# Kernel optimization log

Hardware: AMD Instinct MI355X
Metric: run time of the kernel (lower is better)

## Reference

```python
import jax, jax.numpy as jnp
import numpy as np

E = 1024; H = 16; L = 4; V = 32000; FF = 4096
B = 2; NX = 1023; S = 1024
EPS = 1e-5


def _pe(n_pos, d):
    # sinusoidal table; original registers pe of shape [max_len, 1, d]
    pos = np.arange(n_pos, dtype=np.float32)[:, None]
    div = np.exp(np.arange(0, d, 2, dtype=np.float32) * (-np.log(10000.0) / d))
    pe = np.zeros((n_pos, d), dtype=np.float32)
    pe[:, 0::2] = np.sin(pos * div)
    pe[:, 1::2] = np.cos(pos * div)
    return jnp.asarray(pe)


def _ln(x, g, b):
    m = jnp.mean(x, -1, keepdims=True)
    v = jnp.mean((x - m) ** 2, -1, keepdims=True)
    return (x - m) / jnp.sqrt(v + EPS) * g + b


def _mha(q, k, v, Wq, bq, Wk, bk, Wv, bv, Wo, bo, mask=None):
    b, lq, e = q.shape
    hd = e // H
    qh = (q @ Wq + bq).reshape(b, lq, H, hd)
    kh = (k @ Wk + bk).reshape(b, k.shape[1], H, hd)
    vh = (v @ Wv + bv).reshape(b, v.shape[1], H, hd)
    s = jnp.einsum('bqhe,bkhe->bhqk', qh, kh)
    if mask is not None:
        s = jnp.where(mask == 0, -1e9, s)  # mask applied BEFORE scaling, as in source
    s = s / np.float32(np.sqrt(e))        # quirk: scaled by sqrt(embed_size), not head_size
    a = jax.nn.softmax(s, axis=-1)
    o = jnp.einsum('bhqk,bkhd->bqhd', a, vh).reshape(b, lq, e)
    return o @ Wo + bo


def _forward(emb, cls, sWq, sbq, sWk, sbk, sWv, sbv, sWo, sbo,
             cWq, cbq, cWk, cbk, cWv, cbv, cWo, cbo,
             g1, b1, g2, b2, g3, b3, fW1, fb1, fW2, fb2, x_tok, y_tok):
    scale = np.float32(np.sqrt(E))
    # quirk: original adds pe[:x.size(0)] (batch dim!) broadcast over sequence
    pe = _pe(x_tok.shape[0], E)
    x = emb[x_tok] * scale + pe[:, None, :]
    y = emb[y_tok] * scale + pe[:, None, :]
    s = y_tok.shape[1]
    mask = jnp.tril(jnp.ones((s, s), jnp.float32))[None, None]  # [1,1,s,s] causal
    x = jnp.concatenate([x, jnp.broadcast_to(cls, (x.shape[0], 1, E))], axis=1)
    for l in range(L):
        # quirk: every layer self-attends over the ORIGINAL embedded y
        a1 = _mha(y, y, y, sWq[l], sbq[l], sWk[l], sbk[l], sWv[l], sbv[l], sWo[l], sbo[l], mask)
        yl = _ln(y + a1, g1[l], b1[l])
        a2 = _mha(yl, x, x, cWq[l], cbq[l], cWk[l], cbk[l], cWv[l], cbv[l], cWo[l], cbo[l])
        x = _ln(yl + a2, g2[l], b2[l])
        h = jax.nn.relu(x @ fW1[l] + fb1[l]) @ fW2[l] + fb2[l]
        x = _ln(x + h, g3[l], b3[l])
    return x


def setup_inputs() -> dict:
    key = jax.random.key(0)
    specs = [('emb', (V, E), 1.0), ('cls', (1, 1, E), 1.0),
             ('sWq', (L, E, E), 0.02), ('sbq', (L, E), 0.01), ('sWk', (L, E, E), 0.02), ('sbk', (L, E), 0.01),
             ('sWv', (L, E, E), 0.02), ('sbv', (L, E), 0.01), ('sWo', (L, E, E), 0.02), ('sbo', (L, E), 0.01),
             ('cWq', (L, E, E), 0.02), ('cbq', (L, E), 0.01), ('cWk', (L, E, E), 0.02), ('cbk', (L, E), 0.01),
             ('cWv', (L, E, E), 0.02), ('cbv', (L, E), 0.01), ('cWo', (L, E, E), 0.02), ('cbo', (L, E), 0.01),
             ('fW1', (L, E, FF), 0.02), ('fb1', (L, FF), 0.01), ('fW2', (L, FF, E), 0.02), ('fb2', (L, E), 0.01)]
    d = {}
    for i, (n, sh, sc) in enumerate(specs):
        d[n] = jax.random.normal(jax.random.fold_in(key, i), sh, jnp.float32) * sc
    for n in ('g1', 'g2', 'g3'):
        d[n] = jnp.ones((L, E), jnp.float32)
    for n in ('b1', 'b2', 'b3'):
        d[n] = jnp.zeros((L, E), jnp.float32)
    d['x_tok'] = jax.random.randint(jax.random.fold_in(key, 100), (B, NX), 0, V)
    d['y_tok'] = jax.random.randint(jax.random.fold_in(key, 101), (B, S), 0, V)
    return d


def reference(x_tok, y_tok, emb, cls, sWq, sbq, sWk, sbk, sWv, sbv, sWo, sbo,
              cWq, cbq, cWk, cbk, cWv, cbv, cWo, cbo,
              g1, b1, g2, b2, g3, b3, fW1, fb1, fW2, fb2):
    return _forward(emb, cls, sWq, sbq, sWk, sbk, sWv, sbv, sWo, sbo,
                    cWq, cbq, cWk, cbk, cWv, cbv, cWo, cbo,
                    g1, b1, g2, b2, g3, b3, fW1, fb1, fW2, fb2, x_tok, y_tok)
```

## Files before the change

kernel.cpp:

```cpp
#include <hip/hip_runtime.h>
#include <cstdint>

#define ESZ 1024
#define NH 16
#define HD 64
#define NLAYER 4
#define FFD 4096
#define NB 2
#define NXTOK 1023
#define SEQ 1024
#define LNEPS 1e-5f

typedef __attribute__((ext_vector_type(8))) _Float16 f16x8;
typedef __attribute__((ext_vector_type(4))) _Float16 f16x4;
typedef __attribute__((ext_vector_type(4))) float f32x4;

__device__ __forceinline__ void gld16(const void* g, void* l) {
  __builtin_amdgcn_global_load_lds(
      (const __attribute__((address_space(1))) unsigned int*)g,
      (__attribute__((address_space(3))) unsigned int*)l, 16, 0, 0);
}

__device__ __forceinline__ uint3 xcd_swz() {
  unsigned gx = gridDim.x, gy = gridDim.y;
  unsigned nwg = gx * gy * gridDim.z;
  unsigned lin = (blockIdx.z * gy + blockIdx.y) * gx + blockIdx.x;
  unsigned q = nwg >> 3, r = nwg & 7;
  unsigned xcd = lin & 7, idx = lin >> 3;
  unsigned wid = (xcd < r ? xcd * (q + 1) : r * (q + 1) + (xcd - r) * q) + idx;
  uint3 o;
  o.x = wid % gx;
  unsigned t = wid / gx;
  o.y = t % gy;
  o.z = t / gy;
  return o;
}

template<int MI, int NJ, int EPI, bool RELU, int SPLITK>
__device__ __forceinline__ void gemm_epi(
    f32x4 (&acc)[MI][NJ], int m0, int n0, int wr, int wc, int lr, int hi,
    int z, size_t coff, int ldc,
    const float* bias0, const float* bias1, const float* bias2, int bstr,
    void* C0, void* C1, long sC1, long sC2, int vseg)
{
  const int rb = hi * 4;
#pragma unroll
  for (int j = 0; j < NJ; j++) {
    const int n = n0 + wc + j * 16 + lr;
    float bv = 0.f;
    if (EPI == 2) {
      int seg = n >> 10;
      const float* bp = (seg == 0) ? bias0 : ((seg == 1) ? bias1 : bias2);
      bv = bp[bstr * z + (n & 1023)];
    } else if (bias0) bv = bias0[bstr * z + n];
    if (SPLITK > 1 && z > 0) bv = 0.f;
#pragma unroll
    for (int i = 0; i < MI; i++) {
#pragma unroll
      for (int r = 0; r < 4; r++) {
        int row = m0 + wr + i * 16 + rb + r;
        float out = acc[i][j][r] + bv;
        if (RELU) out = fmaxf(out, 0.f);
        if (EPI == 0) {
          ((float*)C0)[coff + (size_t)row * ldc + n] = out;
        } else if (EPI == 1) {
          ((_Float16*)C0)[coff + (size_t)row * ldc + n] = (_Float16)out;
        } else {
          int seg = n >> 10, n1 = n & 1023, h = n1 >> 6, d = n1 & 63;
          int b = row >> 10, s = row & 1023;
          if (seg == vseg)
            ((_Float16*)C1)[(size_t)z * sC2 + (((size_t)b * NH + h) * HD + d) * SEQ + s] = (_Float16)out;
          else
            ((_Float16*)C0)[(size_t)z * sC1 + (size_t)seg * ((size_t)NB * NH * SEQ * HD)
                            + (((size_t)b * NH + h) * SEQ + s) * HD + d] = (_Float16)out;
        }
      }
    }
  }
}

template<int BM, int BN, int EPI, bool RELU, int SPLITK>
__global__ __launch_bounds__(256)
void gemm_k(const _Float16* __restrict__ A, const _Float16* __restrict__ Bm,
            const float* __restrict__ bias0, const float* __restrict__ bias1,
            const float* __restrict__ bias2,
            void* __restrict__ C0, void* __restrict__ C1,
            int K, int lda, int ldb, int ldc,
            long sAz, long sBz, int cdiv, long sC1, long sC2, int vseg, int bstr)
{
  constexpr int MI = BM / 32, NJ = BN / 32;
  constexpr int DBUF = 2 * (BM + BN) * 64;
  constexpr int TBUF = (EPI == 2) ? 128 * 136 : 0;
  constexpr int LDSN = (TBUF > DBUF) ? TBUF : DBUF;
  __shared__ _Float16 lds[LDSN];

  const uint3 bi = xcd_swz();
  const int m0 = bi.x * BM;
  const int n0 = bi.y * BN;
  const int z = bi.z;
  const _Float16* Ab;
  const _Float16* Bb;
  size_t coff;
  if (SPLITK > 1) {
    int koff = z * (K / SPLITK);
    Ab = A + koff;
    Bb = Bm + koff;
    coff = (size_t)z * sC1;
  } else {
    Ab = A + (size_t)z * sAz;
    Bb = Bm + (size_t)z * sBz;
    coff = (size_t)(z / cdiv) * sC1 + (size_t)(z % cdiv) * sC2;
  }
  const int tid = threadIdx.x;
  const int lane = tid & 63;
  const int w = tid >> 6;
  const int lr = lane & 15;
  const int hi = lane >> 4;
  const int wr = (w >> 1) * (BM / 2);
  const int wc = (w & 1) * (BN / 2);

  const f32x4 vz = {0.f, 0.f, 0.f, 0.f};
  f32x4 acc[MI][NJ];
#pragma unroll
  for (int i = 0; i < MI; i++)
#pragma unroll
    for (int j = 0; j < NJ; j++) acc[i][j] = vz;

  const int nk = (K / SPLITK) >> 6;

  auto stage = [&](int buf, int kt) {
    const int k0 = kt << 6;
    _Float16* Ah = lds + buf * (BM * 64);
    _Float16* Bh = lds + 2 * (BM * 64) + buf * (BN * 64);
#pragma unroll
    for (int c = 0; c < MI; c++) {
      int r = w * (BM / 4) + c * 8 + (lane >> 3);
      int cg = ((lane & 7) ^ (r & 7)) << 3;
      gld16(Ab + (size_t)(m0 + r) * lda + k0 + cg, Ah + (w * (BM / 4) + c * 8) * 64);
    }
#pragma unroll
    for (int c = 0; c < NJ; c++) {
      int r = w * (BN / 4) + c * 8 + (lane >> 3);
      int cg = ((lane & 7) ^ (r & 7)) << 3;
      gld16(Bb + (size_t)(n0 + r) * ldb + k0 + cg, Bh + (w * (BN / 4) + c * 8) * 64);
    }
  };

  stage(0, 0);
  int cur = 0;
  for (int kt = 0; kt < nk; ++kt) {
    __syncthreads();
    if (kt + 1 < nk) stage(cur ^ 1, kt + 1);
    const char* Ah = (const char*)(lds + cur * (BM * 64));
    const char* Bh = (const char*)(lds + 2 * (BM * 64) + cur * (BN * 64));
#pragma unroll
    for (int kk = 0; kk < 2; kk++) {
      f16x8 af[MI], bf[NJ];
#pragma unroll
      for (int i = 0; i < MI; i++) {
        int row = wr + i * 16 + lr;
        int off = ((kk << 6) | (hi << 4)) ^ ((row & 7) << 4);
        af[i] = *(const f16x8*)(Ah + row * 128 + off);
      }
#pragma unroll
      for (int j = 0; j < NJ; j++) {
        int row = wc + j * 16 + lr;
        int off = ((kk << 6) | (hi << 4)) ^ ((row & 7) << 4);
        bf[j] = *(const f16x8*)(Bh + row * 128 + off);
      }
#pragma unroll
      for (int i = 0; i < MI; i++)
#pragma unroll
        for (int j = 0; j < NJ; j++)
          acc[i][j] = __builtin_amdgcn_mfma_f32_16x16x32_f16(af[i], bf[j], acc[i][j], 0, 0, 0);
    }
    cur ^= 1;
  }

  if (EPI == 2 && (n0 >> 10) == vseg) {
    __syncthreads();
    _Float16* T = lds;
    const float* bp = (vseg == 0) ? bias0 : ((vseg == 1) ? bias1 : bias2);
#pragma unroll
    for (int j = 0; j < NJ; j++) {
      int nloc = wc + j * 16 + lr;
      float bv = bp[bstr * z + ((n0 + nloc) & 1023)];
#pragma unroll
      for (int i = 0; i < MI; i++) {
        f16x4 tv;
#pragma unroll
        for (int r = 0; r < 4; r++) tv[r] = (_Float16)(acc[i][j][r] + bv);
        *(f16x4*)(T + nloc * 136 + wr + i * 16 + hi * 4) = tv;
      }
    }
    __syncthreads();
    int rowT = tid >> 1;
    int c0 = (tid & 1) << 6;
    int nn = (n0 & 1023) + rowT;
    int h = nn >> 6, d = nn & 63;
    int bb = m0 >> 10;
    int s0 = (m0 & 1023) + c0;
    _Float16* dst = (_Float16*)C1 + (size_t)z * sC2
                  + (((size_t)bb * NH + h) * HD + d) * SEQ + s0;
    const _Float16* src = T + rowT * 136 + c0;
#pragma unroll
    for (int t2 = 0; t2 < 8; t2++)
      *(f16x8*)(dst + t2 * 8) = *(const f16x8*)(src + t2 * 8);
    return;
  }

  gemm_epi<MI, NJ, EPI, RELU, SPLITK>(acc, m0, n0, wr, wc, lr, hi, z, coff, ldc,
                                      bias0, bias1, bias2, bstr, C0, C1, sC1, sC2, vseg);
}

template<bool CAUSAL>
__global__ __launch_bounds__(256)
void flash_k(const _Float16* __restrict__ qh, const _Float16* __restrict__ kh,
             const _Float16* __restrict__ vTp, _Float16* __restrict__ ob,
             long qs, long ks, long vs, long os)
{
  __shared__ _Float16 Kl[2][64 * 64];
  __shared__ _Float16 Vl[2][64 * 64];
  const uint3 bi = xcd_swz();
  const int qb = bi.x;
  const int bh = bi.y;
  const int layer = bi.z;
  const int b = bh >> 4, h = bh & 15;
  const int q0 = qb * 128;
  const int tid = threadIdx.x;
  const int w = tid >> 6, lane = tid & 63;
  const int lr = lane & 15, hi = lane >> 4;
  const int qw = q0 + w * 32;

  const _Float16* Qp = qh + (size_t)layer * qs + (size_t)bh * SEQ * HD;
  const _Float16* Kp = kh + (size_t)layer * ks + (size_t)bh * SEQ * HD;
  const _Float16* Vp = vTp + (size_t)layer * vs + (size_t)bh * HD * SEQ;
  ob += (size_t)layer * os;

  f16x8 qf[2][2];
#pragma unroll
  for (int jq = 0; jq < 2; jq++)
#pragma unroll
    for (int ds = 0; ds < 2; ds++)
      qf[jq][ds] = *(const f16x8*)(Qp + (size_t)(qw + jq * 16 + lr) * HD + ds * 32 + hi * 8);

  float m[2] = {-1e30f, -1e30f}, l[2] = {0.f, 0.f};
  const f32x4 vz = {0.f, 0.f, 0.f, 0.f};
  f32x4 o[4][2];
#pragma unroll
  for (int dt = 0; dt < 4; dt++)
#pragma unroll
    for (int jq = 0; jq < 2; jq++) o[dt][jq] = vz;

  const int nst = CAUSAL ? ((q0 >> 6) + 2) : (SEQ / 64);

  auto stage = [&](int buf, int kt) {
    const int k0 = kt << 6;
#pragma unroll
    for (int c = 0; c < 2; c++) {
      int r = w * 16 + c * 8 + (lane >> 3);
      int cg = ((lane & 7) ^ (r & 7)) << 3;
      gld16(Kp + (size_t)(k0 + r) * HD + cg, &Kl[buf][(w * 16 + c * 8) * 64]);
      gld16(Vp + (size_t)r * SEQ + k0 + cg, &Vl[buf][(w * 16 + c * 8) * 64]);
    }
  };

  stage(0, 0);
  int cur = 0;
  for (int kt = 0; kt < nst; ++kt) {
    __syncthreads();
    if (kt + 1 < nst) stage(cur ^ 1, kt + 1);
    const int k0 = kt << 6;
    if (!CAUSAL || k0 <= qw + 31) {
      f32x4 s[4][2];
#pragma unroll
      for (int ik = 0; ik < 4; ik++)
#pragma unroll
        for (int jq = 0; jq < 2; jq++) s[ik][jq] = vz;
#pragma unroll
      for (int ds = 0; ds < 2; ds++) {
        f16x8 kf[4];
#pragma unroll
        for (int ik = 0; ik < 4; ik++) {
          int row = ik * 16 + lr;
          int off = (ds * 64 + hi * 16) ^ ((row & 7) << 4);
          kf[ik] = *(const f16x8*)((const char*)&Kl[cur][0] + row * 128 + off);
        }
        __builtin_amdgcn_s_setprio(1);
#pragma unroll
        for (int ik = 0; ik < 4; ik++)
#pragma unroll
          for (int jq = 0; jq < 2; jq++)
            s[ik][jq] = __builtin_amdgcn_mfma_f32_16x16x32_f16(kf[ik], qf[jq][ds], s[ik][jq], 0, 0, 0);
        __builtin_amdgcn_s_setprio(0);
      }
      float mx[2] = {-1e30f, -1e30f};
#pragma unroll
      for (int ik = 0; ik < 4; ik++)
#pragma unroll
        for (int jq = 0; jq < 2; jq++)
#pragma unroll
          for (int r = 0; r < 4; r++) {
            float v = s[ik][jq][r] * 0.03125f;
            if (CAUSAL) {
              int kk = k0 + ik * 16 + hi * 4 + r;
              int qq = qw + jq * 16 + lr;
              if (kk > qq) v = -1e30f;
            }
            s[ik][jq][r] = v;
            mx[jq] = fmaxf(mx[jq], v);
          }
      float sc[2], cs[2] = {0.f, 0.f};
      f16x4 pb[4][2];
#pragma unroll
      for (int jq = 0; jq < 2; jq++) {
        mx[jq] = fmaxf(mx[jq], __shfl_xor(mx[jq], 16, 64));
        mx[jq] = fmaxf(mx[jq], __shfl_xor(mx[jq], 32, 64));
        float mn = fmaxf(m[jq], mx[jq]);
        sc[jq] = __expf(m[jq] - mn);
        m[jq] = mn;
      }
#pragma unroll
      for (int ik = 0; ik < 4; ik++)
#pragma unroll
        for (int jq = 0; jq < 2; jq++)
#pragma unroll
          for (int r = 0; r < 4; r++) {
            float p = __expf(s[ik][jq][r] - m[jq]);
            cs[jq] += p;
            pb[ik][jq][r] = (_Float16)p;
          }
#pragma unroll
      for (int jq = 0; jq < 2; jq++) {
        float t = cs[jq];
        t += __shfl_xor(t, 16, 64);
        t += __shfl_xor(t, 32, 64);
        l[jq] = l[jq] * sc[jq] + t;
      }
#pragma unroll
      for (int dt = 0; dt < 4; dt++)
#pragma unroll
        for (int jq = 0; jq < 2; jq++)
#pragma unroll
          for (int r = 0; r < 4; r++) o[dt][jq][r] *= sc[jq];
#pragma unroll
      for (int ks2 = 0; ks2 < 4; ks2++) {
        f16x4 va[4];
#pragma unroll
        for (int dt = 0; dt < 4; dt++) {
          int row = dt * 16 + lr;
          int off = (ks2 * 32 + hi * 8) ^ ((row & 7) << 4);
          va[dt] = *(const f16x4*)((const char*)&Vl[cur][0] + row * 128 + off);
        }
        __builtin_amdgcn_s_setprio(1);
#pragma unroll
        for (int dt = 0; dt < 4; dt++)
#pragma unroll
          for (int jq = 0; jq < 2; jq++)
            o[dt][jq] = __builtin_amdgcn_mfma_f32_16x16x16f16(va[dt], pb[ks2][jq], o[dt][jq], 0, 0, 0);
        __builtin_amdgcn_s_setprio(0);
      }
    }
    cur ^= 1;
  }

  float inv[2] = {1.f / l[0], 1.f / l[1]};
#pragma unroll
  for (int jq = 0; jq < 2; jq++) {
    int q = qw + jq * 16 + lr;
    size_t rowoff = (size_t)(b * SEQ + q) * ESZ + h * 64;
#pragma unroll
    for (int dt = 0; dt < 4; dt++) {
      f16x4 ov;
#pragma unroll
      for (int r = 0; r < 4; r++) ov[r] = (_Float16)(o[dt][jq][r] * inv[jq]);
      *(f16x4*)(ob + rowoff + dt * 16 + hi * 4) = ov;
    }
  }
}

__device__ __forceinline__ void wtr4(const float* __restrict__ src,
                                     _Float16* __restrict__ dst,
                                     int K, int Ns, int k0, int n0, int tid,
                                     float* T )
{
  const int w = tid >> 6, lane = tid & 63;
#pragma unroll
  for (int rr = 0; rr < 8; rr++) {
    int r = w * 8 + rr;
    const float* s = src + (size_t)(k0 + r) * Ns + n0;
    gld16(s + lane * 4, T + r * 512);
    gld16(s + 256 + lane * 4, T + r * 512 + 256);
  }
  __syncthreads();
#pragma unroll
  for (int pass = 0; pass < 2; pass++) {
    int n = pass * 256 + tid;
    float vv[32];
#pragma unroll
    for (int kk = 0; kk < 32; kk++) vv[kk] = T[kk * 512 + n];
    _Float16* d = dst + (size_t)(n0 + n) * K + k0;
#pragma unroll
    for (int c = 0; c < 4; c++) {
      f16x8 o;
#pragma unroll
      for (int i = 0; i < 8; i++) o[i] = (_Float16)vv[c * 8 + i];
      *(f16x8*)(d + c * 8) = o;
    }
  }
  __syncthreads();
}

struct W8 { const float* p[8]; };

__global__ __launch_bounds__(256)
void prep_k(W8 w8, const float* __restrict__ fW1, const float* __restrict__ fW2,
            _Float16* __restrict__ W16,
            const int* __restrict__ xt, const int* __restrict__ yt,
            const float* __restrict__ emb, const float* __restrict__ cls,
            float* __restrict__ y32, _Float16* __restrict__ y16,
            _Float16* __restrict__ x16)
{
  __shared__ float T[32 * 512];
  const size_t MM = (size_t)1 << 20;
  int idx = blockIdx.x;
  int tid = threadIdx.x;
  if (idx < 2048) {
    int z = idx >> 6, rem = idx & 63;
    int widx = z >> 2, layer = z & 3;
    const float* src = w8.p[widx] + (size_t)layer * (ESZ * ESZ);
    _Float16* dst = W16 + (size_t)layer * 16 * MM + (size_t)widx * MM;
    wtr4(src, dst, 1024, 1024, (rem & 31) * 32, (rem >> 5) * 512, tid, T);
    return;
  }
  if (idx < 3072) {
    int i = idx - 2048;
    int z = i >> 8, rem = i & 255;
    wtr4(fW1 + (size_t)z * ESZ * FFD, W16 + (size_t)z * 16 * MM + 8 * MM,
         1024, 4096, (rem & 31) * 32, (rem >> 5) * 512, tid, T);
    return;
  }
  if (idx < 4096) {
    int i = idx - 3072;
    int z = i >> 8, rem = i & 255;
    wtr4(fW2 + (size_t)z * ESZ * FFD, W16 + (size_t)z * 16 * MM + 12 * MM,
         4096, 1024, (rem & 127) * 32, (rem >> 7) * 512, tid, T);
    return;
  }
  int row = idx - 4096;
  bool isx = row < NB * SEQ;
  int rr = isx ? row : row - NB * SEQ;
  int b = rr >> 10, tpos = rr & (SEQ - 1);
  int col0 = tid * 4;
  float v[4];
  if (isx && tpos == SEQ - 1) {
#pragma unroll
    for (int j = 0; j < 4; j++) v[j] = cls[col0 + j];
  } else {
    int tok = isx ? xt[b * NXTOK + tpos] : yt[b * SEQ + tpos];
    const float* erow = emb + (size_t)tok * ESZ;
#pragma unroll
    for (int j = 0; j < 4; j++) {
      int e = col0 + j;
      float div = expf((float)(e & ~1) * (-9.210340371976184f / 1024.f));
      float ang = (float)b * div;
      float pe = (e & 1) ? cosf(ang) : sinf(ang);
      v[j] = erow[e] * 32.f + pe;
    }
  }
  size_t off = (size_t)rr * ESZ + col0;
  if (isx) {
#pragma unroll
    for (int j = 0; j < 4; j++) x16[off + j] = (_Float16)v[j];
  } else {
#pragma unroll
    for (int j = 0; j < 4; j++) { y32[off + j] = v[j]; y16[off + j] = (_Float16)v[j]; }
  }
}

template<int NP>
__global__ __launch_bounds__(256)
void lnres_k(const float* __restrict__ a, const _Float16* __restrict__ r0,
             const _Float16* __restrict__ r1, const _Float16* __restrict__ r2,
             const _Float16* __restrict__ r3,
             const float* __restrict__ g, const float* __restrict__ b,
             float* __restrict__ o32, _Float16* __restrict__ o16,
             long aStr, long rStr, long oStr, int gStr)
{
  int row = blockIdx.x;
  int lz = blockIdx.y;
  a += (size_t)lz * aStr;
  r0 += (size_t)lz * rStr;
  o32 += (size_t)lz * oStr;
  o16 += (size_t)lz * oStr;
  g += (size_t)lz * gStr;
  b += (size_t)lz * gStr;
  size_t off = (size_t)row * ESZ;
  int tid = threadIdx.x;
  float4 va = *(const float4*)(a + off + tid * 4);
  float x[4] = {va.x, va.y, va.z, va.w};
  {
    f16x4 v = *(const f16x4*)(r0 + off + tid * 4);
#pragma unroll
    for (int j = 0; j < 4; j++) x[j] += (float)v[j];
  }
  if (NP >= 2) {
    f16x4 v = *(const f16x4*)(r1 + off + tid * 4);
#pragma unroll
    for (int j = 0; j < 4; j++) x[j] += (float)v[j];
  }
  if (NP >= 4) {
    f16x4 v = *(const f16x4*)(r2 + off + tid * 4);
    f16x4 u = *(const f16x4*)(r3 + off + tid * 4);
#pragma unroll
    for (int j = 0; j < 4; j++) x[j] += (float)v[j] + (float)u[j];
  }
  float s = x[0] + x[1] + x[2] + x[3];
  float s2 = x[0] * x[0] + x[1] * x[1] + x[2] * x[2] + x[3] * x[3];
  for (int o = 32; o > 0; o >>= 1) {
    s += __shfl_xor(s, o, 64);
    s2 += __shfl_xor(s2, o, 64);
  }
  __shared__ float rs[4], rs2[4];
  if ((tid & 63) == 0) { rs[tid >> 6] = s; rs2[tid >> 6] = s2; }
  __syncthreads();
  s = rs[0] + rs[1] + rs[2] + rs[3];
  s2 = rs2[0] + rs2[1] + rs2[2] + rs2[3];
  float mean = s * (1.f / ESZ);
  float var = s2 * (1.f / ESZ) - mean * mean;
  float inv = 1.f / sqrtf(var + LNEPS);
  float4 vo;
#pragma unroll
  for (int j = 0; j < 4; j++) {
    int c = tid * 4 + j;
    float o = (x[j] - mean) * inv * g[c] + b[c];
    ((float*)&vo)[j] = o;
    o16[off + c] = (_Float16)o;
  }
  *(float4*)(o32 + off + tid * 4) = vo;
}


template<int BM, int BN, int EPI, bool RELU, int SPLITK>
static void gemm(hipStream_t st, const _Float16* A, const _Float16* B,
                 const float* b0, const float* b1, const float* b2,
                 void* C0, void* C1, int M, int N, int K,
                 int lda, int ldb, int ldc,
                 int Z, long sAz, long sBz, int cdiv, long sC1, long sC2,
                 int vseg, int bstr)
{
  dim3 g(M / BM, N / BN, Z);
  gemm_k<BM, BN, EPI, RELU, SPLITK><<<g, dim3(256), 0, st>>>(
      A, B, b0, b1, b2, C0, C1, K, lda, ldb, ldc, sAz, sBz, cdiv, sC1, sC2, vseg, bstr);
}

extern "C" void kernel_launch(void* const* d_in, const int* in_sizes, int n_in,
                              void* d_out, int out_size, void* d_ws, size_t ws_size,
                              hipStream_t stream) {
  (void)n_in; (void)out_size; (void)ws_size;
  const float *emb, *cls, *sWq, *sbq, *sWk, *sbk, *sWv, *sbv, *sWo, *sbo;
  const float *cWq, *cbq, *cWk, *cbk, *cWv, *cbv, *cWo, *cbo;
  const float *fW1, *fb1, *fW2, *fb2, *g1, *g2, *g3, *b1, *b2, *b3;
  const int *xt, *yt;
  if (in_sizes[0] == NB * NXTOK) {
    xt = (const int*)d_in[0]; yt = (const int*)d_in[1];
    emb = (const float*)d_in[2]; cls = (const float*)d_in[3];
    sWq = (const float*)d_in[4]; sbq = (const float*)d_in[5];
    sWk = (const float*)d_in[6]; sbk = (const float*)d_in[7];
    sWv = (const float*)d_in[8]; sbv = (const float*)d_in[9];
    sWo = (const float*)d_in[10]; sbo = (const float*)d_in[11];
    cWq = (const float*)d_in[12]; cbq = (const float*)d_in[13];
    cWk = (const float*)d_in[14]; cbk = (const float*)d_in[15];
    cWv = (const float*)d_in[16]; cbv = (const float*)d_in[17];
    cWo = (const float*)d_in[18]; cbo = (const float*)d_in[19];
    g1 = (const float*)d_in[20]; b1 = (const float*)d_in[21];
    g2 = (const float*)d_in[22]; b2 = (const float*)d_in[23];
    g3 = (const float*)d_in[24]; b3 = (const float*)d_in[25];
    fW1 = (const float*)d_in[26]; fb1 = (const float*)d_in[27];
    fW2 = (const float*)d_in[28]; fb2 = (const float*)d_in[29];
  } else {
    emb = (const float*)d_in[0]; cls = (const float*)d_in[1];
    sWq = (const float*)d_in[2]; sbq = (const float*)d_in[3];
    sWk = (const float*)d_in[4]; sbk = (const float*)d_in[5];
    sWv = (const float*)d_in[6]; sbv = (const float*)d_in[7];
    sWo = (const float*)d_in[8]; sbo = (const float*)d_in[9];
    cWq = (const float*)d_in[10]; cbq = (const float*)d_in[11];
    cWk = (const float*)d_in[12]; cbk = (const float*)d_in[13];
    cWv = (const float*)d_in[14]; cbv = (const float*)d_in[15];
    cWo = (const float*)d_in[16]; cbo = (const float*)d_in[17];
    fW1 = (const float*)d_in[18]; fb1 = (const float*)d_in[19];
    fW2 = (const float*)d_in[20]; fb2 = (const float*)d_in[21];
    g1 = (const float*)d_in[22]; g2 = (const float*)d_in[23]; g3 = (const float*)d_in[24];
    b1 = (const float*)d_in[25]; b2 = (const float*)d_in[26]; b3 = (const float*)d_in[27];
    xt = (const int*)d_in[28]; yt = (const int*)d_in[29];
  }

  const size_t MM = (size_t)1 << 20;
  _Float16* W16 = (_Float16*)d_ws;
  _Float16* qhk_all = W16 + 64 * MM;
  _Float16* vT_all  = W16 + 80 * MM;
  _Float16* ob_all  = W16 + 88 * MM;
  _Float16* y16     = W16 + 96 * MM;
  _Float16* yl16_all= W16 + 98 * MM;
  _Float16* cqh_all = W16 + 106 * MM;
  _Float16* kh_c    = W16 + 114 * MM;
  _Float16* vT_c    = W16 + 116 * MM;
  _Float16* ob_c    = W16 + 118 * MM;
  _Float16* x16     = W16 + 120 * MM;
  _Float16* ffn     = W16 + 122 * MM;
  float* y32      = (float*)(W16 + 130 * MM);
  _Float16* tmp16 = (_Float16*)(y32 + 2 * MM);
  float* yl32_all = y32 + 10 * MM;
  float* x32      = y32 + 18 * MM;
  const long SP16 = 2048L * 1024;

  W8 w8;
  w8.p[0] = sWq; w8.p[1] = sWk; w8.p[2] = sWv; w8.p[3] = cWq;
  w8.p[4] = cWk; w8.p[5] = cWv; w8.p[6] = sWo; w8.p[7] = cWo;
  prep_k<<<dim3(8192), 256, 0, stream>>>(w8, fW1, fW2, W16, xt, yt, emb, cls,
                                         y32, y16, x16);

  gemm<128, 128, 2, false, 1>(stream, y16, W16, sbq, sbk, sbv,
      qhk_all, vT_all, 2048, 3072, 1024, 1024, 1024, 0,
      4, 0, 16 * MM, 1, 4 * MM, 2 * MM, 2, 1024);
  flash_k<true><<<dim3(8, 32, 4), 256, 0, stream>>>(
      qhk_all, qhk_all + 2 * MM, vT_all, ob_all, 4 * MM, 4 * MM, 2 * MM, 2 * MM);
  gemm<128, 128, 1, false, 1>(stream, ob_all, W16 + 6 * MM, sbo, nullptr, nullptr,
      tmp16, nullptr, 2048, 1024, 1024, 1024, 1024, 1024,
      4, 2 * MM, 16 * MM, 1, SP16, 0, 0, 1024);
  lnres_k<1><<<dim3(2048, 4), 256, 0, stream>>>(y32, tmp16, nullptr, nullptr, nullptr,
      g1, b1, yl32_all, yl16_all, 0, SP16, 2 * MM, 1024);
  gemm<128, 128, 2, false, 1>(stream, yl16_all, W16 + 3 * MM, cbq, nullptr, nullptr,
      cqh_all, nullptr, 2048, 1024, 1024, 1024, 1024, 0,
      4, 2 * MM, 16 * MM, 1, 2 * MM, 0, 3, 1024);

  for (int l = 0; l < NLAYER; l++) {
    _Float16* wl   = W16 + (size_t)l * 16 * MM;
    _Float16* wckv = wl + 4 * MM;
    _Float16* wco  = wl + 7 * MM;
    _Float16* wf1  = wl + 8 * MM;
    _Float16* wf2  = wl + 12 * MM;

    gemm<128, 128, 2, false, 1>(stream, x16, wckv, cbk + l * ESZ, cbv + l * ESZ,
        nullptr, kh_c, vT_c, 2048, 2048, 1024, 1024, 1024, 0,
        1, 0, 0, 1, 0, 0, 1, 0);
    flash_k<false><<<dim3(8, 32, 1), 256, 0, stream>>>(
        cqh_all + (size_t)l * 2 * MM, kh_c, vT_c, ob_c, 0, 0, 0, 0);
    gemm<128, 128, 1, false, 2>(stream, ob_c, wco, cbo + l * ESZ, nullptr, nullptr,
        tmp16, nullptr, 2048, 1024, 1024, 1024, 1024, 1024,
        2, 0, 0, 1, SP16, 0, 0, 0);
    lnres_k<2><<<dim3(2048, 1), 256, 0, stream>>>(yl32_all + (size_t)l * 2 * MM,
        tmp16, tmp16 + SP16, nullptr, nullptr,
        g2 + l * ESZ, b2 + l * ESZ, x32, x16, 0, 0, 0, 0);

    gemm<128, 128, 1, true, 1>(stream, x16, wf1, fb1 + l * FFD, nullptr, nullptr,
        ffn, nullptr, 2048, 4096, 1024, 1024, 1024, 4096,
        1, 0, 0, 1, 0, 0, 0, 0);
    gemm<128, 128, 1, false, 4>(stream, ffn, wf2, fb2 + l * ESZ, nullptr, nullptr,
        tmp16, nullptr, 2048, 1024, 4096, 4096, 4096, 1024,
        4, 0, 0, 1, SP16, 0, 0, 0);
    lnres_k<4><<<dim3(2048, 1), 256, 0, stream>>>(x32, tmp16, tmp16 + SP16,
        tmp16 + 2 * SP16, tmp16 + 3 * SP16, g3 + l * ESZ, b3 + l * ESZ,
        (l == NLAYER - 1) ? (float*)d_out : x32, x16, 0, 0, 0, 0);
  }
}
```

Before: 814.9 us.

## Pre-tile transposed fp16 weights into contiguous 128x64 blocks for GEMM B loads

The weight-prep kernel now writes each transposed fp16 weight as contiguous 128(N)x64(K) tiles, so each 64-wide K step of a GEMM block's B operand is one 16 KB contiguous chunk. The GEMM B-stage addressing is changed to match this blocked layout, including the split-K offset. This is meant to make B global loads fully sequential and simplify prep-kernel transposes with smaller LDS tiles, at the cost of more prep blocks. The layout assumes BN=128 and would break for other B tile widths or for any GEMM whose B operand is not a pre-tiled weight.

```diff
diff --git a/kernel.cpp b/kernel.cpp
--- a/kernel.cpp
+++ b/kernel.cpp
@@ -104,7 +104,7 @@
   if (SPLITK > 1) {
     int koff = z * (K / SPLITK);
     Ab = A + koff;
-    Bb = Bm + koff;
+    Bb = Bm + (size_t)koff * 128;
     coff = (size_t)z * sC1;
   } else {
     Ab = A + (size_t)z * sAz;
@@ -118,6 +118,7 @@
   const int hi = lane >> 4;
   const int wr = (w >> 1) * (BM / 2);
   const int wc = (w & 1) * (BN / 2);
+  const size_t nblk = (size_t)(n0 >> 7) * 128 * (size_t)ldb;
 
   const f32x4 vz = {0.f, 0.f, 0.f, 0.f};
   f32x4 acc[MI][NJ];
@@ -142,7 +143,8 @@
     for (int c = 0; c < NJ; c++) {
       int r = w * (BN / 4) + c * 8 + (lane >> 3);
       int cg = ((lane & 7) ^ (r & 7)) << 3;
-      gld16(Bb + (size_t)(n0 + r) * ldb + k0 + cg, Bh + (w * (BN / 4) + c * 8) * 64);
+      gld16(Bb + nblk + ((size_t)kt << 13) + (size_t)r * 64 + cg,
+            Bh + (w * (BN / 4) + c * 8) * 64);
     }
   };
 
@@ -379,36 +381,32 @@
   }
 }
 
-__device__ __forceinline__ void wtr4(const float* __restrict__ src,
-                                     _Float16* __restrict__ dst,
-                                     int K, int Ns, int k0, int n0, int tid,
+__device__ __forceinline__ void wtr6(const float* __restrict__ src,
+                                     _Float16* __restrict__ dstT,
+                                     int Ns, int k0, int n0, int tid,
                                      float* T )
 {
   const int w = tid >> 6, lane = tid & 63;
 #pragma unroll
-  for (int rr = 0; rr < 8; rr++) {
-    int r = w * 8 + rr;
-    const float* s = src + (size_t)(k0 + r) * Ns + n0;
-    gld16(s + lane * 4, T + r * 512);
-    gld16(s + 256 + lane * 4, T + r * 512 + 256);
+  for (int c = 0; c < 8; c++) {
+    int rbase = w * 16 + c * 2;
+    int r = rbase + (lane >> 5);
+    gld16(src + (size_t)(k0 + r) * Ns + n0 + (lane & 31) * 4, T + rbase * 128);
   }
   __syncthreads();
-#pragma unroll
-  for (int pass = 0; pass < 2; pass++) {
-    int n = pass * 256 + tid;
-    float vv[32];
-#pragma unroll
-    for (int kk = 0; kk < 32; kk++) vv[kk] = T[kk * 512 + n];
-    _Float16* d = dst + (size_t)(n0 + n) * K + k0;
-#pragma unroll
-    for (int c = 0; c < 4; c++) {
-      f16x8 o;
-#pragma unroll
-      for (int i = 0; i < 8; i++) o[i] = (_Float16)vv[c * 8 + i];
-      *(f16x8*)(d + c * 8) = o;
-    }
-  }
-  __syncthreads();
+  const int n = tid >> 1;
+  const int kh = (tid & 1) * 32;
+  float vv[32];
+#pragma unroll
+  for (int i = 0; i < 32; i++) vv[i] = T[(kh + i) * 128 + n];
+  _Float16* d = dstT + (size_t)n * 64 + kh;
+#pragma unroll
+  for (int c = 0; c < 4; c++) {
+    f16x8 o;
+#pragma unroll
+    for (int i = 0; i < 8; i++) o[i] = (_Float16)vv[c * 8 + i];
+    *(f16x8*)(d + c * 8) = o;
+  }
 }
 
 struct W8 { const float* p[8]; };
@@ -421,33 +419,39 @@
             float* __restrict__ y32, _Float16* __restrict__ y16,
             _Float16* __restrict__ x16)
 {
-  __shared__ float T[32 * 512];
+  __shared__ float T[64 * 128];
   const size_t MM = (size_t)1 << 20;
   int idx = blockIdx.x;
   int tid = threadIdx.x;
-  if (idx < 2048) {
-    int z = idx >> 6, rem = idx & 63;
+  if (idx < 4096) {
+    int z = idx >> 7, rem = idx & 127;
     int widx = z >> 2, layer = z & 3;
+    int kt = rem & 15, nt = rem >> 4;
     const float* src = w8.p[widx] + (size_t)layer * (ESZ * ESZ);
-    _Float16* dst = W16 + (size_t)layer * 16 * MM + (size_t)widx * MM;
-    wtr4(src, dst, 1024, 1024, (rem & 31) * 32, (rem >> 5) * 512, tid, T);
+    _Float16* dst = W16 + (size_t)layer * 16 * MM + (size_t)widx * MM
+                  + (size_t)nt * 131072 + (size_t)kt * 8192;
+    wtr6(src, dst, 1024, kt * 64, nt * 128, tid, T);
     return;
   }
-  if (idx < 3072) {
-    int i = idx - 2048;
-    int z = i >> 8, rem = i & 255;
-    wtr4(fW1 + (size_t)z * ESZ * FFD, W16 + (size_t)z * 16 * MM + 8 * MM,
-         1024, 4096, (rem & 31) * 32, (rem >> 5) * 512, tid, T);
+  if (idx < 6144) {
+    int i = idx - 4096;
+    int z = i >> 9, rem = i & 511;
+    int kt = rem & 15, nt = rem >> 4;
+    _Float16* dst = W16 + (size_t)z * 16 * MM + 8 * MM
+                  + (size_t)nt * 131072 + (size_t)kt * 8192;
+    wtr6(fW1 + (size_t)z * ESZ * FFD, dst, 4096, kt * 64, nt * 128, tid, T);
     return;
   }
-  if (idx < 4096) {
-    int i = idx - 3072;
-    int z = i >> 8, rem = i & 255;
-    wtr4(fW2 + (size_t)z * ESZ * FFD, W16 + (size_t)z * 16 * MM + 12 * MM,
-         4096, 1024, (rem & 127) * 32, (rem >> 7) * 512, tid, T);
+  if (idx < 8192) {
+    int i = idx - 6144;
+    int z = i >> 9, rem = i & 511;
+    int kt = rem & 63, nt = rem >> 6;
+    _Float16* dst = W16 + (size_t)z * 16 * MM + 12 * MM
+                  + (size_t)nt * 524288 + (size_t)kt * 8192;
+    wtr6(fW2 + (size_t)z * ESZ * FFD, dst, 1024, kt * 64, nt * 128, tid, T);
     return;
   }
-  int row = idx - 4096;
+  int row = idx - 8192;
   bool isx = row < NB * SEQ;
   int rr = isx ? row : row - NB * SEQ;
   int b = rr >> 10, tpos = rr & (SEQ - 1);
@@ -617,8 +621,8 @@
   W8 w8;
   w8.p[0] = sWq; w8.p[1] = sWk; w8.p[2] = sWv; w8.p[3] = cWq;
   w8.p[4] = cWk; w8.p[5] = cWv; w8.p[6] = sWo; w8.p[7] = cWo;
-  prep_k<<<dim3(8192), 256, 0, stream>>>(w8, fW1, fW2, W16, xt, yt, emb, cls,
-                                         y32, y16, x16);
+  prep_k<<<dim3(12288), 256, 0, stream>>>(w8, fW1, fW2, W16, xt, yt, emb, cls,
+                                          y32, y16, x16);
 
   gemm<128, 128, 2, false, 1>(stream, y16, W16, sbq, sbk, sbv,
       qhk_all, vT_all, 2048, 3072, 1024, 1024, 1024, 0,
```

Result: faster. 794.8 us (-2.5%).
